# Kernel tuning notes

Measured on AMD Instinct MI355X. Metric: run time of the kernel, lower is better.

## Reference

```python
import math
import jax, jax.numpy as jnp
import numpy as np

EPS = 1e-5
DIM_E = 448
DIM_H = 64
TOTAL = DIM_E + DIM_H  # 512
C = 1.0


def _project(x, c, margin=1e-3):
    sqrt_c = jnp.sqrt(c)
    norm = jnp.maximum(jnp.linalg.norm(x, axis=-1, keepdims=True), EPS)
    scale = jnp.minimum(((1.0 - margin) / sqrt_c) / norm, 1.0)
    return x * scale


def _mobius_add(x, y, c):
    x2 = jnp.sum(x * x, axis=-1, keepdims=True)
    y2 = jnp.sum(y * y, axis=-1, keepdims=True)
    xy = jnp.sum(x * y, axis=-1, keepdims=True)
    num = (1.0 + 2.0 * c * xy + c * y2) * x + (1.0 - c * x2) * y
    den = jnp.maximum(1.0 + 2.0 * c * xy + c * c * x2 * y2, EPS)
    return _project(num / den, c)


def _exp0(v, c):
    sqrt_c = jnp.sqrt(c)
    norm = jnp.maximum(jnp.linalg.norm(v, axis=-1, keepdims=True), EPS)
    return _project(jnp.tanh(sqrt_c * norm) * v / (sqrt_c * norm), c)


def _dist(x, y, c):
    # x, y broadcast to [B,S,S,dim_h]; returns [B,S,S]
    sqrt_c = jnp.sqrt(c)
    diff = _mobius_add(-x, y, c)
    norm = jnp.minimum(jnp.linalg.norm(diff, axis=-1), (1.0 - 1e-5) / sqrt_c)
    return (2.0 / sqrt_c) * jnp.arctanh(jnp.minimum(sqrt_c * norm, 1.0 - 1e-5))


def setup_inputs() -> dict:
    key = jax.random.key(0)
    ks = jax.random.split(key, 10)
    B, S = 1, 1024
    s = 1.0 / math.sqrt(TOTAL)
    inp = {
        "x": jax.random.normal(ks[0], (B, S, TOTAL), jnp.float32),
        "wq": jax.random.uniform(ks[1], (TOTAL, TOTAL), jnp.float32, -s, s),
        "bq": jax.random.uniform(ks[2], (TOTAL,), jnp.float32, -s, s),
        "wk": jax.random.uniform(ks[3], (TOTAL, TOTAL), jnp.float32, -s, s),
        "bk": jax.random.uniform(ks[4], (TOTAL,), jnp.float32, -s, s),
        "wv": jax.random.uniform(ks[5], (TOTAL, TOTAL), jnp.float32, -s, s),
        "bv": jax.random.uniform(ks[6], (TOTAL,), jnp.float32, -s, s),
        "wo": jax.random.uniform(ks[7], (TOTAL, TOTAL), jnp.float32, -s, s),
        "bo": jax.random.uniform(ks[8], (TOTAL,), jnp.float32, -s, s),
        "alpha_unconstrained": jnp.float32(0.0),
    }
    return inp


def reference(x, wq, bq, wk, bk, wv, bv, wo, bo, alpha_unconstrained):
    q = x @ wq.T + bq
    k = x @ wk.T + bk
    v = x @ wv.T + bv
    qe, qh = q[..., :DIM_E], q[..., DIM_E:]
    ke, kh = k[..., :DIM_E], k[..., DIM_E:]
    # Euclidean squared distance [B,S,S] via GEMM expansion
    qn = jnp.sum(qe * qe, axis=-1)  # [B,S]
    kn = jnp.sum(ke * ke, axis=-1)  # [B,S]
    d_e = qn[:, :, None] + kn[:, None, :] - 2.0 * jnp.einsum("bsd,btd->bst", qe, ke)
    # Hyperbolic distance on Poincare ball
    qh_h = _exp0(qh, C)
    kh_h = _exp0(kh, C)
    d_h = _dist(qh_h[:, :, None, :], kh_h[:, None, :, :], C)  # [B,S,S]
    alpha = jax.nn.softplus(alpha_unconstrained)
    dist = d_e + alpha * d_h * d_h
    logits = jnp.clip(-dist / math.sqrt(float(TOTAL)), -50.0, 0.0)
    attn = jax.nn.softmax(logits, axis=-1)
    out = jnp.einsum("bst,btd->bsd", attn, v)
    return out @ wo.T + bo
```

## Files before the change

kernel.cpp:

```cpp
#include <hip/hip_runtime.h>

#define S_LEN 1024
#define D_TOT 512
#define D_E   448

typedef short bf16x8 __attribute__((ext_vector_type(8)));
typedef float f32x4  __attribute__((ext_vector_type(4)));
typedef unsigned short u16;

__device__ __forceinline__ float frcp(float x) {
  float r; asm("v_rcp_f32 %0, %1" : "=v"(r) : "v"(x)); return r;
}

__device__ __forceinline__ float wave_sum64(float v) {
#pragma unroll
  for (int o = 32; o > 0; o >>= 1) v += __shfl_xor(v, o);
  return v;
}

__device__ __forceinline__ u16 bf16rne(float f) {
  unsigned u = __builtin_bit_cast(unsigned, f);
  return (u16)((u + 0x7fffu + ((u >> 16) & 1u)) >> 16);
}

__device__ __forceinline__ void bsplit(float f, u16 &h, u16 &l) {
  unsigned u  = __builtin_bit_cast(unsigned, f);
  unsigned ur = u + 0x7fffu + ((u >> 16) & 1u);
  h = (u16)(ur >> 16);
  float fh = __builtin_bit_cast(float, ur & 0xffff0000u);
  float r  = f - fh;
  l = bf16rne(r);
}

__device__ __forceinline__ void bsplit8(float4 a, float4 b, uint4 &h, uint4 &l) {
  u16 h0,h1,h2,h3,h4,h5,h6,h7, l0,l1,l2,l3,l4,l5,l6,l7;
  bsplit(a.x,h0,l0); bsplit(a.y,h1,l1); bsplit(a.z,h2,l2); bsplit(a.w,h3,l3);
  bsplit(b.x,h4,l4); bsplit(b.y,h5,l5); bsplit(b.z,h6,l6); bsplit(b.w,h7,l7);
  h.x = (unsigned)h0 | ((unsigned)h1<<16); h.y = (unsigned)h2 | ((unsigned)h3<<16);
  h.z = (unsigned)h4 | ((unsigned)h5<<16); h.w = (unsigned)h6 | ((unsigned)h7<<16);
  l.x = (unsigned)l0 | ((unsigned)l1<<16); l.y = (unsigned)l2 | ((unsigned)l3<<16);
  l.z = (unsigned)l4 | ((unsigned)l5<<16); l.w = (unsigned)l6 | ((unsigned)l7<<16);
}

__device__ __forceinline__ uint4 rne8(float4 a, float4 b) {
  uint4 h;
  h.x = (unsigned)bf16rne(a.x) | ((unsigned)bf16rne(a.y)<<16);
  h.y = (unsigned)bf16rne(a.z) | ((unsigned)bf16rne(a.w)<<16);
  h.z = (unsigned)bf16rne(b.x) | ((unsigned)bf16rne(b.y)<<16);
  h.w = (unsigned)bf16rne(b.z) | ((unsigned)bf16rne(b.w)<<16);
  return h;
}

#define MFMA2(ACC)                                                                              \
  _Pragma("unroll") for (int i_ = 0; i_ < 2; ++i_)                                              \
  _Pragma("unroll") for (int j_ = 0; j_ < 2; ++j_) {                                            \
    ACC[i_][j_] = __builtin_amdgcn_mfma_f32_16x16x32_bf16(fAh[i_], fBh[j_], ACC[i_][j_],0,0,0); \
    ACC[i_][j_] = __builtin_amdgcn_mfma_f32_16x16x32_bf16(fAh[i_], fBl[j_], ACC[i_][j_],0,0,0); \
  }

#define MFMA1(ACC)                                                                              \
  _Pragma("unroll") for (int i_ = 0; i_ < 2; ++i_)                                              \
  _Pragma("unroll") for (int j_ = 0; j_ < 2; ++j_)                                              \
    ACC[i_][j_] = __builtin_amdgcn_mfma_f32_16x16x32_bf16(fAh[i_], fBh[j_], ACC[i_][j_],0,0,0);

__global__ __launch_bounds__(512,4) void qkv_mfma(
    const float* __restrict__ x,
    const float* __restrict__ wq, const float* __restrict__ bq,
    const float* __restrict__ wk, const float* __restrict__ bk,
    const float* __restrict__ wv, const float* __restrict__ bv,
    u16* __restrict__ Qch, u16* __restrict__ Kch, u16* __restrict__ vTh,
    float* __restrict__ qnpart, float* __restrict__ knpart,
    float* __restrict__ uh2a, float* __restrict__ vh2a)
{
  __shared__ __align__(16) u16 stage[2][15360];
  float* fbuf = (float*)stage;
  const int z = blockIdx.z;
  const float* W; const float* bias;
  if (z == 0)      { W = wq; bias = bq; }
  else if (z == 1) { W = wk; bias = bk; }
  else             { W = wv; bias = bv; }
  const int mBase = blockIdx.y << 6, nBase = blockIdx.x << 6;
  const int t = threadIdx.x, lane = t & 63, wave = t >> 6;
  const int kg = t >> 8, sub = t & 255;
  const int srow = sub >> 2, scol = (sub & 3) << 3;
  const int kgw = wave >> 2, wr = (wave >> 1) & 1, wc = wave & 1;

  const float* Ag = x + (size_t)(mBase + srow) * D_TOT + scol + kg * 256;
  const float* Bg = W + (size_t)(nBase + srow) * D_TOT + scol + kg * 256;

  const int sb = kg * 7680 + srow * 40 + scol;
  const int fa = kgw * 7680 + (wr * 32 + (lane & 15)) * 40 + ((lane >> 4) << 3);
  const int fb = kgw * 7680 + 2560 + (wc * 32 + (lane & 15)) * 40 + ((lane >> 4) << 3);

  float4 a0 = *(const float4*)Ag, a1 = *(const float4*)(Ag + 4);
  float4 b0 = *(const float4*)Bg, b1 = *(const float4*)(Bg + 4);
  {
    uint4 hB,lB; bsplit8(b0,b1,hB,lB);
    *(uint4*)&stage[0][sb       ] = rne8(a0,a1);
    *(uint4*)&stage[0][sb + 2560] = hB;
    *(uint4*)&stage[0][sb + 5120] = lB;
  }
  a0 = *(const float4*)(Ag + 32); a1 = *(const float4*)(Ag + 36);
  b0 = *(const float4*)(Bg + 32); b1 = *(const float4*)(Bg + 36);

  f32x4 zero = {0.f,0.f,0.f,0.f};
  f32x4 acc[2][2] = {{zero,zero},{zero,zero}};
#pragma unroll
  for (int r = 0; r < 8; ++r) {
    __syncthreads();
    const u16* bufr = stage[r & 1];
    bf16x8 fAh[2], fBh[2], fBl[2];
#pragma unroll
    for (int i = 0; i < 2; ++i) {
      fAh[i] = *(const bf16x8*)&bufr[fa        + i*640];
      fBh[i] = *(const bf16x8*)&bufr[fb        + i*640];
      fBl[i] = *(const bf16x8*)&bufr[fb + 2560 + i*640];
    }
    if (r + 1 < 8) {
      u16* bufw = stage[(r + 1) & 1];
      uint4 hB,lB; bsplit8(b0,b1,hB,lB);
      *(uint4*)&bufw[sb       ] = rne8(a0,a1);
      *(uint4*)&bufw[sb + 2560] = hB;
      *(uint4*)&bufw[sb + 5120] = lB;
      if (r + 2 < 8) {
        const int o = (r + 2) * 32;
        a0 = *(const float4*)(Ag + o); a1 = *(const float4*)(Ag + o + 4);
        b0 = *(const float4*)(Bg + o); b1 = *(const float4*)(Bg + o + 4);
      }
    }
    MFMA2(acc);
  }

  __syncthreads();
  {
    const int r0 = wr*32 + ((lane>>4)<<2);
    const int c0 = wc*32 + (lane&15);
#pragma unroll
    for (int i = 0; i < 2; ++i)
#pragma unroll
      for (int j = 0; j < 2; ++j)
#pragma unroll
        for (int g = 0; g < 4; ++g)
          fbuf[kgw*4352 + (r0 + i*16 + g)*68 + c0 + j*16] = acc[i][j][g];
  }
  __syncthreads();
  const int erow = wave << 3;
  float val[8];
  {
    const float b = bias[nBase + lane];
#pragma unroll
    for (int r = 0; r < 8; ++r)
      val[r] = fbuf[(erow+r)*68 + lane] + fbuf[4352 + (erow+r)*68 + lane] + b;
  }

  if (z == 2) {
    u16 hh[8];
#pragma unroll
    for (int r = 0; r < 8; ++r) hh[r] = bf16rne(val[r]);
    const size_t off = (size_t)(nBase + lane) * S_LEN + mBase + erow;
    ushort4 p0{hh[0],hh[1],hh[2],hh[3]}, p1{hh[4],hh[5],hh[6],hh[7]};
    *(ushort4*)(vTh + off) = p0; *(ushort4*)(vTh + off + 4) = p1;
  } else {
    u16* Ch = z ? Kch : Qch;
    float* np_ = z ? knpart : qnpart;
    float* u2a = z ? vh2a  : uh2a;
    if (blockIdx.x < 7) {
#pragma unroll
      for (int r = 0; r < 8; ++r) {
        const int s = mBase + erow + r;
        Ch[(size_t)s*D_TOT + nBase + lane] = bf16rne(val[r]);
        float p = wave_sum64(val[r]*val[r]);
        if (lane == 0) np_[s*8 + blockIdx.x] = p;
      }
    } else {
#pragma unroll
      for (int r = 0; r < 8; ++r) {
        const int s = mBase + erow + r;
        float n2 = wave_sum64(val[r]*val[r]);
        float nn = sqrtf(n2);
        float n  = fmaxf(nn, 1e-5f);
        float e2n = __expf(2.f*n);
        float th  = 1.f - 2.f*frcp(e2n + 1.f);
        float rn  = frcp(n);
        float pn  = th * nn * rn;
        float scale = fminf(0.999f * frcp(fmaxf(pn, 1e-5f)), 1.f);
        float u = th * rn * scale * val[r];
        float un = pn * scale;
        Ch[(size_t)s*D_TOT + nBase + lane] = bf16rne(u);
        if (lane == 0) u2a[s] = un*un;
      }
    }
  }
}

__global__ __launch_bounds__(512,4) void score_mfma(
    const u16* __restrict__ Qch, const u16* __restrict__ Kch,
    const float* __restrict__ qnpart, const float* __restrict__ knpart,
    const float* __restrict__ uh2a, const float* __restrict__ vh2a,
    const float* __restrict__ alpha_u,
    u16* __restrict__ Eh, float* __restrict__ rowpart)
{
  __shared__ __align__(16) char shm_[69632];
  __shared__ float rowscal[256];
  u16* stg = (u16*)shm_;
  float* fbuf = (float*)shm_;
  const int t = threadIdx.x, lane = t & 63, wave = t >> 6;
  const int mBase = blockIdx.y << 6, nBase = blockIdx.x << 6;
  if (t < 64) {
    float s_ = 0.f;
#pragma unroll
    for (int c = 0; c < 7; ++c) s_ += qnpart[(mBase+t)*8 + c];
    rowscal[t] = s_;
  } else if (t < 128) {
    float s_ = 0.f;
#pragma unroll
    for (int c = 0; c < 7; ++c) s_ += knpart[(nBase+t-64)*8 + c];
    rowscal[t] = s_;
  } else if (t < 192) rowscal[t] = uh2a[mBase + t - 128];
  else if (t < 256)   rowscal[t] = vh2a[nBase + t - 192];

  const int kg = t >> 8, sub = t & 255;
  const int srow = sub >> 2, scol = (sub & 3) << 3;
  const int kgw = wave >> 2, wr = (wave >> 1) & 1, wc = wave & 1;
  const u16* Agh = Qch + (size_t)(mBase+srow)*D_TOT + scol;
  const u16* Bgh = Kch + (size_t)(nBase+srow)*D_TOT + scol;

  const int sb  = kg * 5120 + srow * 40 + scol;
  const int fa  = kgw * 5120 + (wr * 32 + (lane & 15)) * 40 + ((lane >> 4) << 3);
  const int fbh = kgw * 5120 + 2560 + (wc * 32 + (lane & 15)) * 40 + ((lane >> 4) << 3);

  int kb = kg * 224;
  uint4 rAh = *(const uint4*)(Agh + kb);
  uint4 rBh = *(const uint4*)(Bgh + kb);
  *(uint4*)&stg[sb       ] = rAh;
  *(uint4*)&stg[sb + 2560] = rBh;
  kb = kg * 224 + 32;
  rAh = *(const uint4*)(Agh + kb);
  rBh = *(const uint4*)(Bgh + kb);

  f32x4 zero = {0.f,0.f,0.f,0.f};
  f32x4 accE[2][2] = {{zero,zero},{zero,zero}};
  f32x4 accH[2][2] = {{zero,zero},{zero,zero}};
#pragma unroll
  for (int r = 0; r < 8; ++r) {
    __syncthreads();
    const u16* bufr = stg + (r & 1) * 10240;
    bf16x8 fAh[2], fBh[2];
#pragma unroll
    for (int i = 0; i < 2; ++i) {
      fAh[i] = *(const bf16x8*)&bufr[fa  + i*640];
      fBh[i] = *(const bf16x8*)&bufr[fbh + i*640];
    }
    if (r + 1 < 8) {
      u16* bufw = stg + ((r + 1) & 1) * 10240;
      *(uint4*)&bufw[sb       ] = rAh;
      *(uint4*)&bufw[sb + 2560] = rBh;
      if (r + 2 < 8) {
        const int o = (r + 2 < 7) ? (kg*224 + (r+2)*32) : (448 + kg*32);
        rAh = *(const uint4*)(Agh + o);
        rBh = *(const uint4*)(Bgh + o);
      }
    }
    if (r < 7) { MFMA1(accE) } else { MFMA1(accH) }
  }

  __syncthreads();
  {
    const int r0 = wr*32 + ((lane>>4)<<2);
    const int c0 = wc*32 + (lane&15);
#pragma unroll
    for (int i = 0; i < 2; ++i)
#pragma unroll
      for (int j = 0; j < 2; ++j)
#pragma unroll
        for (int g = 0; g < 4; ++g) {
          fbuf[       kgw*4352 + (r0 + i*16 + g)*68 + c0 + j*16] = accE[i][j][g];
          fbuf[8704 + kgw*4352 + (r0 + i*16 + g)*68 + c0 + j*16] = accH[i][j][g];
        }
  }
  __syncthreads();
  const int erow = wave << 3;
  float eE[8], eH[8];
#pragma unroll
  for (int r = 0; r < 8; ++r) {
    eE[r] = fbuf[(erow+r)*68 + lane] + fbuf[4352 + (erow+r)*68 + lane];
    eH[r] = fbuf[8704 + (erow+r)*68 + lane] + fbuf[8704 + 4352 + (erow+r)*68 + lane];
  }

  const float alpha = __logf(1.f + __expf(alpha_u[0]));
  const float inv_s = 0.04419417382415922f;
  const float knl = rowscal[64 + lane], v2 = rowscal[192 + lane];
#pragma unroll
  for (int r = 0; r < 8; ++r) {
    const int s = mBase + erow + r;
    const float qns = rowscal[erow + r], u2 = rowscal[128 + erow + r];
    float de   = qns + knl - 2.f * eE[r];
    float dH   = eH[r];
    float Ac   = 1.f - 2.f*dH + v2;
    float Bc   = 1.f - u2;
    float num2 = Ac*Ac*u2 + Bc*Bc*v2 - 2.f*Ac*Bc*dH;
    float den  = fmaxf(1.f - 2.f*dH + u2*v2, 1e-5f);
    float frac = sqrtf(fmaxf(num2, 0.f)) * frcp(den);
    float nrm  = fminf(frac, 0.999f);
    float dh_  = __logf((1.f + nrm) * frcp(1.f - nrm));
    float dist = de + alpha * dh_ * dh_;
    float lg   = fminf(fmaxf(-dist * inv_s, -50.f), 0.f);
    float e    = __expf(lg);
    Eh[(size_t)s*S_LEN + nBase + lane] = bf16rne(e);
    float rs = wave_sum64(e);
    if (lane == 0) rowpart[s*16 + blockIdx.x] = rs;
  }
}

__global__ __launch_bounds__(512,4) void av_mfma(
    const u16* __restrict__ Eh, const u16* __restrict__ vTh,
    const float* __restrict__ rowpart,
    u16* __restrict__ out1h)
{
  __shared__ __align__(16) u16 stage[2][15360];
  __shared__ float rinvl[32];
  float* fbuf = (float*)stage;
  const int t = threadIdx.x, lane = t & 63, wave = t >> 6;
  const int mBase = blockIdx.y << 5, nBase = blockIdx.x << 6;
  if (t < 32) {
    float s_ = 0.f;
#pragma unroll
    for (int c = 0; c < 16; ++c) s_ += rowpart[(mBase+t)*16 + c];
    rinvl[t] = 1.f / s_;
  }
  const int kg = t >> 7, sub = t & 127;
  const int arow = sub >> 2, acol = (sub & 3) << 3;
  const int brow0 = sub >> 2, brow1 = 32 + (sub >> 2), bcol = (sub & 3) << 3;
  const int kgw = wave >> 1, wc = wave & 1;

  const u16* Ag = Eh  + (size_t)(mBase+arow)*S_LEN + kg*256 + acol;
  const u16* B0 = vTh + (size_t)(nBase+brow0)*S_LEN + kg*256 + bcol;
  const u16* B1 = vTh + (size_t)(nBase+brow1)*S_LEN + kg*256 + bcol;

  const int sA  = kg*3840 + arow*40 + acol;
  const int sB0 = kg*3840 + 1280 + brow0*40 + bcol;
  const int sB1 = kg*3840 + 1280 + brow1*40 + bcol;
  const int fa  = kgw*3840 + (lane&15)*40 + ((lane>>4)<<3);
  const int fb  = kgw*3840 + 1280 + (wc*32 + (lane&15))*40 + ((lane>>4)<<3);

  uint4 rA = *(const uint4*)Ag;
  uint4 rb0 = *(const uint4*)B0, rb1 = *(const uint4*)B1;
  *(uint4*)&stage[0][sA ] = rA;
  *(uint4*)&stage[0][sB0] = rb0; *(uint4*)&stage[0][sB1] = rb1;
  rA = *(const uint4*)(Ag + 32);
  rb0 = *(const uint4*)(B0 + 32); rb1 = *(const uint4*)(B1 + 32);

  f32x4 zero = {0.f,0.f,0.f,0.f};
  f32x4 acc[2][2] = {{zero,zero},{zero,zero}};
#pragma unroll
  for (int r = 0; r < 8; ++r) {
    __syncthreads();
    const u16* bufr = stage[r & 1];
    bf16x8 fAh[2], fBh[2];
#pragma unroll
    for (int i = 0; i < 2; ++i) {
      fAh[i] = *(const bf16x8*)&bufr[fa + i*640];
      fBh[i] = *(const bf16x8*)&bufr[fb + i*640];
    }
    if (r + 1 < 8) {
      u16* bufw = stage[(r + 1) & 1];
      *(uint4*)&bufw[sA ] = rA;
      *(uint4*)&bufw[sB0] = rb0; *(uint4*)&bufw[sB1] = rb1;
      if (r + 2 < 8) {
        const int o = (r + 2) * 32;
        rA = *(const uint4*)(Ag + o);
        rb0 = *(const uint4*)(B0 + o); rb1 = *(const uint4*)(B1 + o);
      }
    }
    MFMA1(acc);
  }

  __syncthreads();
  {
    const int r0 = (lane>>4)<<2;
    const int c0 = wc*32 + (lane&15);
#pragma unroll
    for (int i = 0; i < 2; ++i)
#pragma unroll
      for (int j = 0; j < 2; ++j)
#pragma unroll
        for (int g = 0; g < 4; ++g)
          fbuf[kgw*2176 + (r0 + i*16 + g)*68 + c0 + j*16] = acc[i][j][g];
  }
  __syncthreads();
  const int erow = wave << 2;
#pragma unroll
  for (int r = 0; r < 4; ++r) {
    const int row = erow + r;
    float e = fbuf[row*68 + lane] + fbuf[2176 + row*68 + lane]
            + fbuf[4352 + row*68 + lane] + fbuf[6528 + row*68 + lane];
    float v_ = e * rinvl[row];
    const int s = mBase + row;
    out1h[(size_t)s*D_TOT + nBase + lane] = bf16rne(v_);
  }
}

__global__ __launch_bounds__(512,4) void final_mfma(
    const u16* __restrict__ out1h,
    const float* __restrict__ wo, const float* __restrict__ bo,
    float* __restrict__ out)
{
  __shared__ __align__(16) u16 stg[25600];
  float* fbuf = (float*)stg;
  const int t = threadIdx.x, lane = t & 63, wave = t >> 6;
  const int mBase = blockIdx.y << 5, nBase = blockIdx.x << 6;
  const int kg = t >> 7, sub = t & 127;
  const int arow = sub >> 2, acol = (sub & 3) << 3;
  const int brow0 = sub >> 2, bcol0 = (sub & 3) << 3;
  const int brow1 = (sub + 128) >> 2, bcol1 = ((sub + 128) & 3) << 3;
  const int kgw = wave >> 1, wc = wave & 1;

  const u16* Ag = out1h + (size_t)(mBase+arow)*D_TOT + acol + kg*128;
  const float* B0 = wo + (size_t)(nBase+brow0)*D_TOT + bcol0 + kg*128;
  const float* B1 = wo + (size_t)(nBase+brow1)*D_TOT + bcol1 + kg*128;

  const int sA  = kg*6400 + arow*40 + acol;
  const int sB0 = kg*6400 + 1280 + brow0*40 + bcol0;
  const int sB1 = kg*6400 + 1280 + brow1*40 + bcol1;
  const int fa  = kgw*6400 + (lane&15)*40 + ((lane>>4)<<3);
  const int fbh = kgw*6400 + 1280 + (wc*32 + (lane&15))*40 + ((lane>>4)<<3);

  uint4 rA = *(const uint4*)Ag;
  float4 b00 = *(const float4*)B0, b01 = *(const float4*)(B0 + 4);
  float4 b10 = *(const float4*)B1, b11 = *(const float4*)(B1 + 4);

  f32x4 zero = {0.f,0.f,0.f,0.f};
  f32x4 acc[2][2] = {{zero,zero},{zero,zero}};
#pragma unroll
  for (int r = 0; r < 4; ++r) {
    __syncthreads();
    uint4 bh0,bl0,bh1,bl1;
    bsplit8(b00,b01,bh0,bl0); bsplit8(b10,b11,bh1,bl1);
    *(uint4*)&stg[sA        ] = rA;
    *(uint4*)&stg[sB0       ] = bh0; *(uint4*)&stg[sB0 + 2560] = bl0;
    *(uint4*)&stg[sB1       ] = bh1; *(uint4*)&stg[sB1 + 2560] = bl1;
    if (r + 1 < 4) {
      const int o = (r + 1) * 32;
      rA = *(const uint4*)(Ag + o);
      b00 = *(const float4*)(B0 + o); b01 = *(const float4*)(B0 + o + 4);
      b10 = *(const float4*)(B1 + o); b11 = *(const float4*)(B1 + o + 4);
    }
    __syncthreads();
    bf16x8 fAh[2], fBh[2], fBl[2];
#pragma unroll
    for (int i = 0; i < 2; ++i) {
      fAh[i] = *(const bf16x8*)&stg[fa         + i*640];
      fBh[i] = *(const bf16x8*)&stg[fbh        + i*640];
      fBl[i] = *(const bf16x8*)&stg[fbh + 2560 + i*640];
    }
    MFMA2(acc);
  }

  __syncthreads();
  {
    const int r0 = (lane>>4)<<2;
    const int c0 = wc*32 + (lane&15);
#pragma unroll
    for (int i = 0; i < 2; ++i)
#pragma unroll
      for (int j = 0; j < 2; ++j)
#pragma unroll
        for (int g = 0; g < 4; ++g)
          fbuf[kgw*2176 + (r0 + i*16 + g)*68 + c0 + j*16] = acc[i][j][g];
  }
  __syncthreads();
  const int erow = wave << 2;
  const float b = bo[nBase + lane];
#pragma unroll
  for (int r = 0; r < 4; ++r) {
    const int row = erow + r;
    float e = fbuf[row*68 + lane] + fbuf[2176 + row*68 + lane]
            + fbuf[4352 + row*68 + lane] + fbuf[6528 + row*68 + lane];
    out[(size_t)(mBase+row)*D_TOT + nBase + lane] = e + b;
  }
}

extern "C" void kernel_launch(void* const* d_in, const int* in_sizes, int n_in,
                              void* d_out, int out_size, void* d_ws, size_t ws_size,
                              hipStream_t stream)
{
  const float* x   = (const float*)d_in[0];
  const float* wq  = (const float*)d_in[1];
  const float* bq  = (const float*)d_in[2];
  const float* wk  = (const float*)d_in[3];
  const float* bk  = (const float*)d_in[4];
  const float* wv  = (const float*)d_in[5];
  const float* bv  = (const float*)d_in[6];
  const float* wo  = (const float*)d_in[7];
  const float* bo  = (const float*)d_in[8];
  const float* alpha_u = (const float*)d_in[9];
  float* out = (float*)d_out;

  u16* U = (u16*)d_ws;
  u16* Qch   = U + 0;
  u16* Kch   = U + 524288;
  u16* vTh   = U + 1048576;
  u16* Eh    = U + 1572864;
  u16* out1h = U + 2621440;
  float* F = (float*)(U + 3145728);
  float* qnpart  = F;
  float* knpart  = F + 8192;
  float* uh2a    = F + 16384;
  float* vh2a    = F + 17408;
  float* rowpart = F + 18432;

  qkv_mfma<<<dim3(8,16,3), 512, 0, stream>>>(x, wq,bq, wk,bk, wv,bv,
      Qch, Kch, vTh, qnpart, knpart, uh2a, vh2a);
  score_mfma<<<dim3(16,16), 512, 0, stream>>>(Qch, Kch,
      qnpart, knpart, uh2a, vh2a, alpha_u, Eh, rowpart);
  av_mfma<<<dim3(8,32), 512, 0, stream>>>(Eh, vTh, rowpart, out1h);
  final_mfma<<<dim3(8,32), 512, 0, stream>>>(out1h, wo, bo, out);
}
```

Baseline: 38.15 us.

## Drop split-bf16 weight correction and double-buffer the output projection GEMM

The QKV and output projection GEMMs no longer split weights into high and low bf16 parts. Weights are rounded to a single bf16, which halves the MFMA count and the shared-memory staging for B. The final projection kernel also moves from a single buffer with two barriers per step to a double-buffered pipeline with one barrier per step, overlapping global loads with MFMA. The cost is lower precision in the weights, which may widen error against the fp32 reference, especially the distance logits fed to the softmax.

After: 34.59 us (median of 2 runs). 1.1x faster.

```diff
diff --git a/kernel.cpp b/kernel.cpp
--- a/kernel.cpp
+++ b/kernel.cpp
@@ -21,25 +21,6 @@
 __device__ __forceinline__ u16 bf16rne(float f) {
   unsigned u = __builtin_bit_cast(unsigned, f);
   return (u16)((u + 0x7fffu + ((u >> 16) & 1u)) >> 16);
-}
-
-__device__ __forceinline__ void bsplit(float f, u16 &h, u16 &l) {
-  unsigned u  = __builtin_bit_cast(unsigned, f);
-  unsigned ur = u + 0x7fffu + ((u >> 16) & 1u);
-  h = (u16)(ur >> 16);
-  float fh = __builtin_bit_cast(float, ur & 0xffff0000u);
-  float r  = f - fh;
-  l = bf16rne(r);
-}
-
-__device__ __forceinline__ void bsplit8(float4 a, float4 b, uint4 &h, uint4 &l) {
-  u16 h0,h1,h2,h3,h4,h5,h6,h7, l0,l1,l2,l3,l4,l5,l6,l7;
-  bsplit(a.x,h0,l0); bsplit(a.y,h1,l1); bsplit(a.z,h2,l2); bsplit(a.w,h3,l3);
-  bsplit(b.x,h4,l4); bsplit(b.y,h5,l5); bsplit(b.z,h6,l6); bsplit(b.w,h7,l7);
-  h.x = (unsigned)h0 | ((unsigned)h1<<16); h.y = (unsigned)h2 | ((unsigned)h3<<16);
-  h.z = (unsigned)h4 | ((unsigned)h5<<16); h.w = (unsigned)h6 | ((unsigned)h7<<16);
-  l.x = (unsigned)l0 | ((unsigned)l1<<16); l.y = (unsigned)l2 | ((unsigned)l3<<16);
-  l.z = (unsigned)l4 | ((unsigned)l5<<16); l.w = (unsigned)l6 | ((unsigned)l7<<16);
 }
 
 __device__ __forceinline__ uint4 rne8(float4 a, float4 b) {
@@ -50,13 +31,6 @@
   h.w = (unsigned)bf16rne(b.z) | ((unsigned)bf16rne(b.w)<<16);
   return h;
 }
-
-#define MFMA2(ACC)                                                                              \
-  _Pragma("unroll") for (int i_ = 0; i_ < 2; ++i_)                                              \
-  _Pragma("unroll") for (int j_ = 0; j_ < 2; ++j_) {                                            \
-    ACC[i_][j_] = __builtin_amdgcn_mfma_f32_16x16x32_bf16(fAh[i_], fBh[j_], ACC[i_][j_],0,0,0); \
-    ACC[i_][j_] = __builtin_amdgcn_mfma_f32_16x16x32_bf16(fAh[i_], fBl[j_], ACC[i_][j_],0,0,0); \
-  }
 
 #define MFMA1(ACC)                                                                              \
   _Pragma("unroll") for (int i_ = 0; i_ < 2; ++i_)                                              \
@@ -72,7 +46,7 @@
     float* __restrict__ qnpart, float* __restrict__ knpart,
     float* __restrict__ uh2a, float* __restrict__ vh2a)
 {
-  __shared__ __align__(16) u16 stage[2][15360];
+  __shared__ __align__(16) u16 stage[2][10240];
   float* fbuf = (float*)stage;
   const int z = blockIdx.z;
   const float* W; const float* bias;
@@ -88,18 +62,14 @@
   const float* Ag = x + (size_t)(mBase + srow) * D_TOT + scol + kg * 256;
   const float* Bg = W + (size_t)(nBase + srow) * D_TOT + scol + kg * 256;
 
-  const int sb = kg * 7680 + srow * 40 + scol;
-  const int fa = kgw * 7680 + (wr * 32 + (lane & 15)) * 40 + ((lane >> 4) << 3);
-  const int fb = kgw * 7680 + 2560 + (wc * 32 + (lane & 15)) * 40 + ((lane >> 4) << 3);
+  const int sb = kg * 5120 + srow * 40 + scol;
+  const int fa = kgw * 5120 + (wr * 32 + (lane & 15)) * 40 + ((lane >> 4) << 3);
+  const int fb = kgw * 5120 + 2560 + (wc * 32 + (lane & 15)) * 40 + ((lane >> 4) << 3);
 
   float4 a0 = *(const float4*)Ag, a1 = *(const float4*)(Ag + 4);
   float4 b0 = *(const float4*)Bg, b1 = *(const float4*)(Bg + 4);
-  {
-    uint4 hB,lB; bsplit8(b0,b1,hB,lB);
-    *(uint4*)&stage[0][sb       ] = rne8(a0,a1);
-    *(uint4*)&stage[0][sb + 2560] = hB;
-    *(uint4*)&stage[0][sb + 5120] = lB;
-  }
+  *(uint4*)&stage[0][sb       ] = rne8(a0,a1);
+  *(uint4*)&stage[0][sb + 2560] = rne8(b0,b1);
   a0 = *(const float4*)(Ag + 32); a1 = *(const float4*)(Ag + 36);
   b0 = *(const float4*)(Bg + 32); b1 = *(const float4*)(Bg + 36);
 
@@ -109,26 +79,23 @@
   for (int r = 0; r < 8; ++r) {
     __syncthreads();
     const u16* bufr = stage[r & 1];
-    bf16x8 fAh[2], fBh[2], fBl[2];
+    bf16x8 fAh[2], fBh[2];
 #pragma unroll
     for (int i = 0; i < 2; ++i) {
-      fAh[i] = *(const bf16x8*)&bufr[fa        + i*640];
-      fBh[i] = *(const bf16x8*)&bufr[fb        + i*640];
-      fBl[i] = *(const bf16x8*)&bufr[fb + 2560 + i*640];
+      fAh[i] = *(const bf16x8*)&bufr[fa + i*640];
+      fBh[i] = *(const bf16x8*)&bufr[fb + i*640];
     }
     if (r + 1 < 8) {
       u16* bufw = stage[(r + 1) & 1];
-      uint4 hB,lB; bsplit8(b0,b1,hB,lB);
       *(uint4*)&bufw[sb       ] = rne8(a0,a1);
-      *(uint4*)&bufw[sb + 2560] = hB;
-      *(uint4*)&bufw[sb + 5120] = lB;
+      *(uint4*)&bufw[sb + 2560] = rne8(b0,b1);
       if (r + 2 < 8) {
         const int o = (r + 2) * 32;
         a0 = *(const float4*)(Ag + o); a1 = *(const float4*)(Ag + o + 4);
         b0 = *(const float4*)(Bg + o); b1 = *(const float4*)(Bg + o + 4);
       }
     }
-    MFMA2(acc);
+    MFMA1(acc);
   }
 
   __syncthreads();
@@ -405,55 +372,60 @@
     const float* __restrict__ wo, const float* __restrict__ bo,
     float* __restrict__ out)
 {
-  __shared__ __align__(16) u16 stg[25600];
-  float* fbuf = (float*)stg;
+  __shared__ __align__(16) u16 stage[2][15360];
+  float* fbuf = (float*)stage;
   const int t = threadIdx.x, lane = t & 63, wave = t >> 6;
   const int mBase = blockIdx.y << 5, nBase = blockIdx.x << 6;
   const int kg = t >> 7, sub = t & 127;
   const int arow = sub >> 2, acol = (sub & 3) << 3;
-  const int brow0 = sub >> 2, bcol0 = (sub & 3) << 3;
-  const int brow1 = (sub + 128) >> 2, bcol1 = ((sub + 128) & 3) << 3;
+  const int brow0 = sub >> 2, brow1 = 32 + (sub >> 2), bcol = (sub & 3) << 3;
   const int kgw = wave >> 1, wc = wave & 1;
 
-  const u16* Ag = out1h + (size_t)(mBase+arow)*D_TOT + acol + kg*128;
-  const float* B0 = wo + (size_t)(nBase+brow0)*D_TOT + bcol0 + kg*128;
-  const float* B1 = wo + (size_t)(nBase+brow1)*D_TOT + bcol1 + kg*128;
-
-  const int sA  = kg*6400 + arow*40 + acol;
-  const int sB0 = kg*6400 + 1280 + brow0*40 + bcol0;
-  const int sB1 = kg*6400 + 1280 + brow1*40 + bcol1;
-  const int fa  = kgw*6400 + (lane&15)*40 + ((lane>>4)<<3);
-  const int fbh = kgw*6400 + 1280 + (wc*32 + (lane&15))*40 + ((lane>>4)<<3);
+  const u16*   Ag = out1h + (size_t)(mBase+arow)*D_TOT + kg*128 + acol;
+  const float* B0 = wo + (size_t)(nBase+brow0)*D_TOT + kg*128 + bcol;
+  const float* B1 = wo + (size_t)(nBase+brow1)*D_TOT + kg*128 + bcol;
+
+  const int sA  = kg*3840 + arow*40 + acol;
+  const int sB0 = kg*3840 + 1280 + brow0*40 + bcol;
+  const int sB1 = kg*3840 + 1280 + brow1*40 + bcol;
+  const int fa  = kgw*3840 + (lane&15)*40 + ((lane>>4)<<3);
+  const int fb  = kgw*3840 + 1280 + (wc*32 + (lane&15))*40 + ((lane>>4)<<3);
 
   uint4 rA = *(const uint4*)Ag;
   float4 b00 = *(const float4*)B0, b01 = *(const float4*)(B0 + 4);
   float4 b10 = *(const float4*)B1, b11 = *(const float4*)(B1 + 4);
+  *(uint4*)&stage[0][sA ] = rA;
+  *(uint4*)&stage[0][sB0] = rne8(b00,b01);
+  *(uint4*)&stage[0][sB1] = rne8(b10,b11);
+  rA = *(const uint4*)(Ag + 32);
+  b00 = *(const float4*)(B0 + 32); b01 = *(const float4*)(B0 + 36);
+  b10 = *(const float4*)(B1 + 32); b11 = *(const float4*)(B1 + 36);
 
   f32x4 zero = {0.f,0.f,0.f,0.f};
   f32x4 acc[2][2] = {{zero,zero},{zero,zero}};
 #pragma unroll
   for (int r = 0; r < 4; ++r) {
     __syncthreads();
-    uint4 bh0,bl0,bh1,bl1;
-    bsplit8(b00,b01,bh0,bl0); bsplit8(b10,b11,bh1,bl1);
-    *(uint4*)&stg[sA        ] = rA;
-    *(uint4*)&stg[sB0       ] = bh0; *(uint4*)&stg[sB0 + 2560] = bl0;
-    *(uint4*)&stg[sB1       ] = bh1; *(uint4*)&stg[sB1 + 2560] = bl1;
+    const u16* bufr = stage[r & 1];
+    bf16x8 fAh[2], fBh[2];
+#pragma unroll
+    for (int i = 0; i < 2; ++i) {
+      fAh[i] = *(const bf16x8*)&bufr[fa + i*640];
+      fBh[i] = *(const bf16x8*)&bufr[fb + i*640];
+    }
     if (r + 1 < 4) {
-      const int o = (r + 1) * 32;
-      rA = *(const uint4*)(Ag + o);
-      b00 = *(const float4*)(B0 + o); b01 = *(const float4*)(B0 + o + 4);
-      b10 = *(const float4*)(B1 + o); b11 = *(const float4*)(B1 + o + 4);
-    }
-    __syncthreads();
-    bf16x8 fAh[2], fBh[2], fBl[2];
-#pragma unroll
-    for (int i = 0; i < 2; ++i) {
-      fAh[i] = *(const bf16x8*)&stg[fa         + i*640];
-      fBh[i] = *(const bf16x8*)&stg[fbh        + i*640];
-      fBl[i] = *(const bf16x8*)&stg[fbh + 2560 + i*640];
-    }
-    MFMA2(acc);
+      u16* bufw = stage[(r + 1) & 1];
+      *(uint4*)&bufw[sA ] = rA;
+      *(uint4*)&bufw[sB0] = rne8(b00,b01);
+      *(uint4*)&bufw[sB1] = rne8(b10,b11);
+      if (r + 2 < 4) {
+        const int o = (r + 2) * 32;
+        rA = *(const uint4*)(Ag + o);
+        b00 = *(const float4*)(B0 + o); b01 = *(const float4*)(B0 + o + 4);
+        b10 = *(const float4*)(B1 + o); b11 = *(const float4*)(B1 + o + 4);
+      }
+    }
+    MFMA1(acc);
   }
 
   __syncthreads();
```
